# Optimization experiments

Hardware: AMD Instinct MI355X
Metric: run time of the kernel (lower is better)

The kernel has to match this reference:

```python
import jax, jax.numpy as jnp
import numpy as np

STRIDE = 1
PADDING = 1


def _ternarize(w):
    # threshold = 0.75 * mean(|w|); alpha = mean(|w| over |w| > threshold)
    abs_w = jnp.abs(w)
    threshold = 0.75 * jnp.mean(abs_w)
    mask = abs_w > threshold
    cnt = jnp.sum(mask)
    alpha = jnp.where(cnt > 0, jnp.sum(jnp.where(mask, abs_w, 0.0)) / jnp.maximum(cnt, 1), 1.0)
    tern = jnp.where(w > threshold, alpha, jnp.where(w < -threshold, -alpha, 0.0))
    # straight-through estimator: forward uses tern, grad flows to w as identity
    return w + jax.lax.stop_gradient(tern - w)


def setup_inputs() -> dict:
    key = jax.random.key(0)
    k_x, k_w = jax.random.split(key)
    x = jax.random.normal(k_x, (32, 256, 56, 56), dtype=jnp.float32)
    weight = jax.random.normal(k_w, (256, 256, 3, 3), dtype=jnp.float32)
    return {"x": x, "weight": weight}


def reference(x, weight):
    tw = _ternarize(weight)
    # NCHW input, OIHW kernel
    return jax.lax.conv_general_dilated(
        x, tw,
        window_strides=(STRIDE, STRIDE),
        padding=[(PADDING, PADDING), (PADDING, PADDING)],
        dimension_numbers=("NCHW", "OIHW", "NCHW"),
    )
```

## Files before the change

### kernel.cpp

```cpp
#include <hip/hip_runtime.h>
#include <hip/hip_bf16.h>

typedef short short8 __attribute__((ext_vector_type(8)));
typedef float f32x4 __attribute__((ext_vector_type(4)));

constexpr int N_  = 32;
constexpr int C_  = 256;
constexpr int K_  = 256;
constexpr int H_  = 56;
constexpr int W_  = 56;
constexpr int HW_ = H_ * W_;
constexpr int NW_ = K_ * C_ * 9;

constexpr int TH   = 4;
constexpr int NB   = 14;
constexpr int HR   = 6, HC = 58;
constexpr int NH   = HR * HC;
constexpr int BROW = 80;
constexpr int BSZ  = NH * BROW;
constexpr int NPAIR2 = 8 * NH;
constexpr int SITER  = 6;
constexpr int ASTEP  = 16384;

constexpr int WS_P1 = 4, WS_P2 = 260, WS_P3 = 516;
constexpr size_t WS_WQ = 4096;
constexpr size_t WS_NEEDED = WS_WQ + (size_t)NW_ * 2;

__device__ __forceinline__ unsigned f2bf(float f) {
    unsigned u = __builtin_bit_cast(unsigned, f);
    return (u + 0x7FFFu + ((u >> 16) & 1u)) >> 16;
}

__global__ void k_abs_partial(const float* __restrict__ w, float* __restrict__ ws) {
    __shared__ float sm[4];
    float s = 0.f;
    for (int i = blockIdx.x * 256 + threadIdx.x; i < NW_; i += 256 * 256)
        s += fabsf(w[i]);
    #pragma unroll
    for (int o = 32; o > 0; o >>= 1) s += __shfl_down(s, o, 64);
    const int wid = threadIdx.x >> 6, lane = threadIdx.x & 63;
    if (lane == 0) sm[wid] = s;
    __syncthreads();
    if (threadIdx.x == 0) {
        float r = 0.f;
        for (int i = 0; i < 4; ++i) r += sm[i];
        ws[WS_P1 + blockIdx.x] = r;
    }
}

__global__ void k_masked_partial(const float* __restrict__ w, float* __restrict__ ws) {
    __shared__ float sm[4];
    float t = ws[WS_P1 + threadIdx.x];
    #pragma unroll
    for (int o = 32; o > 0; o >>= 1) t += __shfl_down(t, o, 64);
    const int wid = threadIdx.x >> 6, lane = threadIdx.x & 63;
    if (lane == 0) sm[wid] = t;
    __syncthreads();
    float total = 0.f;
    for (int i = 0; i < 4; ++i) total += sm[i];
    const float thr = 0.75f * total / (float)NW_;
    if (blockIdx.x == 0 && threadIdx.x == 0) ws[0] = total;
    __syncthreads();
    float s = 0.f, c = 0.f;
    for (int i = blockIdx.x * 256 + threadIdx.x; i < NW_; i += 256 * 256) {
        float a = fabsf(w[i]);
        if (a > thr) { s += a; c += 1.f; }
    }
    #pragma unroll
    for (int o = 32; o > 0; o >>= 1) { s += __shfl_down(s, o, 64); c += __shfl_down(c, o, 64); }
    __shared__ float sm2[8];
    if (lane == 0) { sm2[wid] = s; sm2[wid + 4] = c; }
    __syncthreads();
    if (threadIdx.x == 0) {
        float S = 0.f, C2 = 0.f;
        for (int i = 0; i < 4; ++i) { S += sm2[i]; C2 += sm2[i + 4]; }
        ws[WS_P2 + blockIdx.x] = S;
        ws[WS_P3 + blockIdx.x] = C2;
    }
}

__global__ void k_final_masked(float* __restrict__ ws) {
    __shared__ float sm[8];
    float s = ws[WS_P2 + threadIdx.x];
    float c = ws[WS_P3 + threadIdx.x];
    #pragma unroll
    for (int o = 32; o > 0; o >>= 1) { s += __shfl_down(s, o, 64); c += __shfl_down(c, o, 64); }
    const int wid = threadIdx.x >> 6, lane = threadIdx.x & 63;
    if (lane == 0) { sm[wid] = s; sm[wid + 4] = c; }
    __syncthreads();
    if (threadIdx.x == 0) {
        float S = 0.f, C2 = 0.f;
        for (int i = 0; i < 4; ++i) { S += sm[i]; C2 += sm[i + 4]; }
        ws[1] = S; ws[2] = C2;
    }
}

__device__ __forceinline__ float reduce256_all(const float* __restrict__ p, float* sm) {
    float v = threadIdx.x < 256 ? p[threadIdx.x] : 0.f;
    #pragma unroll
    for (int o = 32; o > 0; o >>= 1) v += __shfl_down(v, o, 64);
    const int wid = threadIdx.x >> 6, lane = threadIdx.x & 63;
    __syncthreads();
    if (lane == 0) sm[wid] = v;
    __syncthreads();
    float total = 0.f;
    #pragma unroll
    for (int i = 0; i < 8; ++i) total += sm[i];
    return total;
}

__global__ __launch_bounds__(512) void k_quant(const float* __restrict__ w,
                                               float* __restrict__ ws,
                                               unsigned short* __restrict__ wq) {
    __shared__ float sm[8];
    const float total = reduce256_all(ws + WS_P1, sm);
    const float msum  = reduce256_all(ws + WS_P2, sm);
    const float mcnt  = reduce256_all(ws + WS_P3, sm);
    const float thr = 0.75f * total / (float)NW_;
    const float alpha = mcnt > 0.f ? msum / fmaxf(mcnt, 1.f) : 1.0f;
    if (blockIdx.x == 0 && threadIdx.x == 0) ws[3] = alpha;
    const int i = blockIdx.x * 512 + threadIdx.x;
    if (i >= NW_) return;
    const float v = w[i];
    const unsigned short q = v > thr ? (unsigned short)0x3F80
                                     : (v < -thr ? (unsigned short)0xBF80 : (unsigned short)0);
    const int k   = i / 2304;
    const int rem = i - k * 2304;
    const int c   = rem / 9;
    const int rs  = rem - c * 9;
    const int chi = c >> 5, c5 = c & 31;
    wq[(size_t)(chi * 9 + rs) * 8192 + (k << 5) + c5] = q;
}

constexpr int RSO_[9] = {
    (0*HC+0)*BROW, (0*HC+1)*BROW, (0*HC+2)*BROW,
    (1*HC+0)*BROW, (1*HC+1)*BROW, (1*HC+2)*BROW,
    (2*HC+0)*BROW, (2*HC+1)*BROW, (2*HC+2)*BROW };

struct ConvState {
    const float* xn;
    const char*  wqc;
    char*        ldsp;
    size_t       aoff;
    int          tid;
    int          bB[7];
    int          xrel[SITER];
    unsigned     okm;
};

__device__ __forceinline__ void load_a(short8 (&d)[4], const ConvState& st, int step) {
    const char* ap = st.wqc + (size_t)step * ASTEP + st.aoff;
    d[0] = *(const short8*)(ap);
    d[1] = *(const short8*)(ap + 1024);
    d[2] = *(const short8*)(ap + 2048);
    d[3] = *(const short8*)(ap + 3072);
}

__device__ __forceinline__ void issue_b(const ConvState& st, int c0, float (&bs)[SITER][4]) {
    #pragma unroll
    for (int it = 0; it < SITER; ++it) {
        const float* p = st.xn + (size_t)c0 * HW_ + st.xrel[it];
        bs[it][0] = p[0];
        bs[it][1] = p[HW_];
        bs[it][2] = p[2 * HW_];
        bs[it][3] = p[3 * HW_];
    }
}

__device__ __forceinline__ void write_b(const ConvState& st, int base,
                                        const float (&bs)[SITER][4]) {
    #pragma unroll
    for (int it = 0; it < SITER; ++it) {
        const int u = it * 512 + st.tid;
        if (u < NPAIR2) {
            const int c4 = u / NH, hidx = u - c4 * NH;
            const bool ok = (st.okm >> it) & 1u;
            const float f0 = ok ? bs[it][0] : 0.f;
            const float f1 = ok ? bs[it][1] : 0.f;
            const float f2 = ok ? bs[it][2] : 0.f;
            const float f3 = ok ? bs[it][3] : 0.f;
            uint2 v;
            v.x = f2bf(f0) | (f2bf(f1) << 16);
            v.y = f2bf(f2) | (f2bf(f3) << 16);
            *(uint2*)(st.ldsp + base + hidx * BROW + c4 * 8) = v;
        }
    }
}

template <int PAR, bool LASTCH>
__device__ __forceinline__ void do_chunk(int chi, const ConvState& st,
                                         short8 (&afr)[2][4], f32x4 (&acc)[4][7],
                                         float (&bs)[SITER][4]) {
    const int rdbase = PAR * BSZ;
    #pragma unroll
    for (int rs = 0; rs < 9; ++rs) {
        const int cur = (PAR + rs) & 1, nxt = cur ^ 1;
        const int step = chi * 9 + rs;
        if (!(LASTCH && rs == 8))
            load_a(afr[nxt], st, step + 1);

        short8 bfr[7];
        #pragma unroll
        for (int nf = 0; nf < 7; ++nf)
            bfr[nf] = *(const short8*)(st.ldsp + rdbase + st.bB[nf] + RSO_[rs]);

        if (rs == 5 && !LASTCH)
            issue_b(st, (chi + 1) * 32, bs);

        if (rs == 8 && !LASTCH) {
            write_b(st, (PAR ^ 1) * BSZ, bs);
            asm volatile("s_waitcnt lgkmcnt(0)" ::: "memory");
            __builtin_amdgcn_s_barrier();
        }

        __builtin_amdgcn_s_setprio(1);
        #pragma unroll
        for (int nf = 0; nf < 7; ++nf)
            #pragma unroll
            for (int mf = 0; mf < 4; ++mf)
                acc[mf][nf] = __builtin_amdgcn_mfma_f32_16x16x32_bf16(
                    afr[cur][mf], bfr[nf], acc[mf][nf], 0, 0, 0);
        __builtin_amdgcn_s_setprio(0);
    }
}

__global__ __launch_bounds__(512, 2) void conv_mfma(const float* __restrict__ x,
                                                    const unsigned short* __restrict__ wq,
                                                    const float* __restrict__ wsc,
                                                    float* __restrict__ out) {
    __shared__ char lds[2 * BSZ];
    const int tid = threadIdx.x, lane = tid & 63, wid = tid >> 6;
    const int wm = wid & 3, wn = wid >> 2, lr = lane & 15, lg = lane >> 4;
    const int band = blockIdx.x, n = blockIdx.y;
    const int h0 = band * TH;

    ConvState st;
    st.xn   = x + (size_t)n * C_ * HW_;
    st.wqc  = (const char*)wq;
    st.ldsp = lds;
    st.aoff = (size_t)(wm * 64 + lr) * 64 + lg * 16;
    st.tid  = tid;
    #pragma unroll
    for (int nf = 0; nf < 7; ++nf) {
        const int pos = wn * 112 + nf * 16 + lr;
        const int y = pos / 56, xx = pos - y * 56;
        st.bB[nf] = (y * HC + xx) * BROW + lg * 16;
    }
    st.okm = 0;
    #pragma unroll
    for (int it = 0; it < SITER; ++it) {
        const int u  = it * 512 + tid;
        const bool vu = u < NPAIR2;
        const int uu = vu ? u : 0;
        const int c4 = uu / NH, hidx = uu - c4 * NH;
        const int hy = hidx / HC, hx = hidx - hy * HC;
        const int h = h0 - 1 + hy, w = hx - 1;
        const bool ok = vu && (unsigned)h < (unsigned)H_ && (unsigned)w < (unsigned)W_;
        st.xrel[it] = ok ? (4 * c4 * HW_ + h * W_ + w) : 0;
        st.okm |= (ok ? 1u : 0u) << it;
    }

    f32x4 acc[4][7] = {};
    short8 afr[2][4];
    float bs[SITER][4];

    issue_b(st, 0, bs);
    load_a(afr[0], st, 0);
    write_b(st, 0, bs);
    asm volatile("s_waitcnt lgkmcnt(0)" ::: "memory");
    __builtin_amdgcn_s_barrier();

    for (int cc = 0; cc < 3; ++cc) {
        do_chunk<0, false>(2 * cc,     st, afr, acc, bs);
        do_chunk<1, false>(2 * cc + 1, st, afr, acc, bs);
    }
    do_chunk<0, false>(6, st, afr, acc, bs);
    do_chunk<1, true >(7, st, afr, acc, bs);

    const float alpha = wsc[3];
    #pragma unroll
    for (int mf = 0; mf < 4; ++mf) {
        const int kb = wm * 64 + mf * 16 + lg * 4;
        #pragma unroll
        for (int j = 0; j < 4; ++j) {
            float* pk = out + ((size_t)n * K_ + (kb + j)) * HW_ + h0 * W_;
            #pragma unroll
            for (int nf = 0; nf < 7; ++nf) {
                const int pos = wn * 112 + nf * 16 + lr;
                pk[pos] = alpha * acc[mf][nf][j];
            }
        }
    }
}

constexpr int W4_ = W_ / 4;
constexpr int SP_ = H_ * W4_;
__global__ __launch_bounds__(256) void conv_tern_otf(const float* __restrict__ x,
                                                     const float* __restrict__ wt,
                                                     const float* __restrict__ wsc,
                                                     float* __restrict__ out) {
    const int kg = blockIdx.x, n = blockIdx.y, k0 = kg * 4;
    const float thr = 0.75f * wsc[0] / (float)NW_;
    const float cnt = wsc[2];
    const float alpha = cnt > 0.f ? wsc[1] / fmaxf(cnt, 1.f) : 1.0f;
    for (int j = 0; j < 4; ++j) {
        const int sp = (int)threadIdx.x + j * 256;
        if (sp >= SP_) break;
        const int h = sp / W4_, w0 = (sp % W4_) * 4;
        float acc[4][4];
        #pragma unroll
        for (int kt = 0; kt < 4; ++kt)
            #pragma unroll
            for (int jj = 0; jj < 4; ++jj) acc[kt][jj] = 0.f;
        for (int c = 0; c < C_; ++c) {
            const float* xp = x + (((size_t)n * C_ + c) * H_) * W_;
            float xr[3][6];
            #pragma unroll
            for (int r = 0; r < 3; ++r) {
                const int hh = h + r - 1;
                const float* rowp = xp + hh * W_;
                if ((unsigned)hh < (unsigned)H_) {
                    const float4 mid = *(const float4*)(rowp + w0);
                    xr[r][1] = mid.x; xr[r][2] = mid.y; xr[r][3] = mid.z; xr[r][4] = mid.w;
                    xr[r][0] = (w0 > 0)      ? rowp[w0 - 1] : 0.f;
                    xr[r][5] = (w0 + 4 < W_) ? rowp[w0 + 4] : 0.f;
                } else {
                    #pragma unroll
                    for (int q = 0; q < 6; ++q) xr[r][q] = 0.f;
                }
            }
            #pragma unroll
            for (int kt = 0; kt < 4; ++kt) {
                const float* wp = wt + ((size_t)(k0 + kt) * C_ + c) * 9;
                #pragma unroll
                for (int r = 0; r < 3; ++r)
                    #pragma unroll
                    for (int s = 0; s < 3; ++s) {
                        float wv = wp[r * 3 + s];
                        wv = wv > thr ? alpha : (wv < -thr ? -alpha : 0.f);
                        #pragma unroll
                        for (int jj = 0; jj < 4; ++jj)
                            acc[kt][jj] = fmaf(wv, xr[r][jj + s], acc[kt][jj]);
                    }
            }
        }
        #pragma unroll
        for (int kt = 0; kt < 4; ++kt) {
            float4 o;
            o.x = acc[kt][0]; o.y = acc[kt][1]; o.z = acc[kt][2]; o.w = acc[kt][3];
            *(float4*)(out + ((((size_t)n * K_ + (k0 + kt)) * H_ + h) * W_ + w0)) = o;
        }
    }
}

extern "C" void kernel_launch(void* const* d_in, const int* in_sizes, int n_in,
                              void* d_out, int out_size, void* d_ws, size_t ws_size,
                              hipStream_t stream) {
    const float* x = (const float*)d_in[0];
    const float* w = (const float*)d_in[1];
    float* out = (float*)d_out;
    float* ws  = (float*)d_ws;
    unsigned short* wq = (unsigned short*)((char*)d_ws + WS_WQ);

    k_abs_partial<<<256, 256, 0, stream>>>(w, ws);
    k_masked_partial<<<256, 256, 0, stream>>>(w, ws);

    if (ws_size >= WS_NEEDED) {
        k_quant<<<(NW_ + 511) / 512, 512, 0, stream>>>(w, ws, wq);
        dim3 grid(NB, N_);
        conv_mfma<<<grid, 512, 0, stream>>>(x, wq, ws, out);
    } else {
        k_final_masked<<<1, 256, 0, stream>>>(ws);
        dim3 grid(64, N_);
        conv_tern_otf<<<grid, 256, 0, stream>>>(x, w, ws, out);
    }
}
```

Before: 138.6 us.

## Fuse masked stats into quant kernel and quad-buffer conv LDS staging

Removes the separate masked-sum pass by having k_quant compute per-block masked sums and counts while quantizing, and moves the alpha reduction into the conv epilogue. The conv kernel switches to four LDS buffers in dynamic shared memory, staging two chunks ahead and placing a barrier only every other chunk, which cuts synchronization. The output store loop is also reordered. The cost is 4x BSZ of LDS per block (about 111KB), which may hurt occupancy at two blocks per CU, plus a per-launch hipFuncSetAttribute call.

```diff
diff --git a/kernel.cpp b/kernel.cpp
--- a/kernel.cpp
+++ b/kernel.cpp
@@ -18,12 +18,16 @@
 constexpr int NH   = HR * HC;
 constexpr int BROW = 80;
 constexpr int BSZ  = NH * BROW;
+constexpr int LDSB = 4 * BSZ;
 constexpr int NPAIR2 = 8 * NH;
 constexpr int SITER  = 6;
 constexpr int ASTEP  = 16384;
 
-constexpr int WS_P1 = 4, WS_P2 = 260, WS_P3 = 516;
-constexpr size_t WS_WQ = 4096;
+constexpr int NQB   = 1152;
+constexpr int WS_P1 = 4;
+constexpr int WS_P2 = 300;
+constexpr int WS_P3 = 1500;
+constexpr size_t WS_WQ = 16384;
 constexpr size_t WS_NEEDED = WS_WQ + (size_t)NW_ * 2;
 
 __device__ __forceinline__ unsigned f2bf(float f) {
@@ -48,53 +52,6 @@
     }
 }
 
-__global__ void k_masked_partial(const float* __restrict__ w, float* __restrict__ ws) {
-    __shared__ float sm[4];
-    float t = ws[WS_P1 + threadIdx.x];
-    #pragma unroll
-    for (int o = 32; o > 0; o >>= 1) t += __shfl_down(t, o, 64);
-    const int wid = threadIdx.x >> 6, lane = threadIdx.x & 63;
-    if (lane == 0) sm[wid] = t;
-    __syncthreads();
-    float total = 0.f;
-    for (int i = 0; i < 4; ++i) total += sm[i];
-    const float thr = 0.75f * total / (float)NW_;
-    if (blockIdx.x == 0 && threadIdx.x == 0) ws[0] = total;
-    __syncthreads();
-    float s = 0.f, c = 0.f;
-    for (int i = blockIdx.x * 256 + threadIdx.x; i < NW_; i += 256 * 256) {
-        float a = fabsf(w[i]);
-        if (a > thr) { s += a; c += 1.f; }
-    }
-    #pragma unroll
-    for (int o = 32; o > 0; o >>= 1) { s += __shfl_down(s, o, 64); c += __shfl_down(c, o, 64); }
-    __shared__ float sm2[8];
-    if (lane == 0) { sm2[wid] = s; sm2[wid + 4] = c; }
-    __syncthreads();
-    if (threadIdx.x == 0) {
-        float S = 0.f, C2 = 0.f;
-        for (int i = 0; i < 4; ++i) { S += sm2[i]; C2 += sm2[i + 4]; }
-        ws[WS_P2 + blockIdx.x] = S;
-        ws[WS_P3 + blockIdx.x] = C2;
-    }
-}
-
-__global__ void k_final_masked(float* __restrict__ ws) {
-    __shared__ float sm[8];
-    float s = ws[WS_P2 + threadIdx.x];
-    float c = ws[WS_P3 + threadIdx.x];
-    #pragma unroll
-    for (int o = 32; o > 0; o >>= 1) { s += __shfl_down(s, o, 64); c += __shfl_down(c, o, 64); }
-    const int wid = threadIdx.x >> 6, lane = threadIdx.x & 63;
-    if (lane == 0) { sm[wid] = s; sm[wid + 4] = c; }
-    __syncthreads();
-    if (threadIdx.x == 0) {
-        float S = 0.f, C2 = 0.f;
-        for (int i = 0; i < 4; ++i) { S += sm[i]; C2 += sm[i + 4]; }
-        ws[1] = S; ws[2] = C2;
-    }
-}
-
 __device__ __forceinline__ float reduce256_all(const float* __restrict__ p, float* sm) {
     float v = threadIdx.x < 256 ? p[threadIdx.x] : 0.f;
     #pragma unroll
@@ -114,13 +71,8 @@
                                                unsigned short* __restrict__ wq) {
     __shared__ float sm[8];
     const float total = reduce256_all(ws + WS_P1, sm);
-    const float msum  = reduce256_all(ws + WS_P2, sm);
-    const float mcnt  = reduce256_all(ws + WS_P3, sm);
     const float thr = 0.75f * total / (float)NW_;
-    const float alpha = mcnt > 0.f ? msum / fmaxf(mcnt, 1.f) : 1.0f;
-    if (blockIdx.x == 0 && threadIdx.x == 0) ws[3] = alpha;
     const int i = blockIdx.x * 512 + threadIdx.x;
-    if (i >= NW_) return;
     const float v = w[i];
     const unsigned short q = v > thr ? (unsigned short)0x3F80
                                      : (v < -thr ? (unsigned short)0xBF80 : (unsigned short)0);
@@ -130,6 +82,74 @@
     const int rs  = rem - c * 9;
     const int chi = c >> 5, c5 = c & 31;
     wq[(size_t)(chi * 9 + rs) * 8192 + (k << 5) + c5] = q;
+    const float a = fabsf(v);
+    float s = a > thr ? a : 0.f;
+    float cn = a > thr ? 1.f : 0.f;
+    #pragma unroll
+    for (int o = 32; o > 0; o >>= 1) { s += __shfl_down(s, o, 64); cn += __shfl_down(cn, o, 64); }
+    __shared__ float sm2[16];
+    const int wid = threadIdx.x >> 6, lane = threadIdx.x & 63;
+    __syncthreads();
+    if (lane == 0) { sm2[wid] = s; sm2[8 + wid] = cn; }
+    __syncthreads();
+    if (threadIdx.x == 0) {
+        float S = 0.f, C2 = 0.f;
+        for (int j = 0; j < 8; ++j) { S += sm2[j]; C2 += sm2[8 + j]; }
+        ws[WS_P2 + blockIdx.x] = S;
+        ws[WS_P3 + blockIdx.x] = C2;
+    }
+}
+
+__global__ void k_fb_total(float* __restrict__ ws) {
+    __shared__ float sm[4];
+    float v = ws[WS_P1 + threadIdx.x];
+    #pragma unroll
+    for (int o = 32; o > 0; o >>= 1) v += __shfl_down(v, o, 64);
+    const int wid = threadIdx.x >> 6, lane = threadIdx.x & 63;
+    if (lane == 0) sm[wid] = v;
+    __syncthreads();
+    if (threadIdx.x == 0) {
+        float r = 0.f;
+        for (int i = 0; i < 4; ++i) r += sm[i];
+        ws[0] = r;
+    }
+}
+
+__global__ void k_fb_masked(const float* __restrict__ w, float* __restrict__ ws) {
+    const float thr = 0.75f * ws[0] / (float)NW_;
+    float s = 0.f, c = 0.f;
+    for (int i = blockIdx.x * 256 + threadIdx.x; i < NW_; i += 256 * 256) {
+        float a = fabsf(w[i]);
+        if (a > thr) { s += a; c += 1.f; }
+    }
+    #pragma unroll
+    for (int o = 32; o > 0; o >>= 1) { s += __shfl_down(s, o, 64); c += __shfl_down(c, o, 64); }
+    __shared__ float sm[8];
+    const int wid = threadIdx.x >> 6, lane = threadIdx.x & 63;
+    if (lane == 0) { sm[wid] = s; sm[4 + wid] = c; }
+    __syncthreads();
+    if (threadIdx.x == 0) {
+        float S = 0.f, C2 = 0.f;
+        for (int i = 0; i < 4; ++i) { S += sm[i]; C2 += sm[i + 4]; }
+        ws[WS_P2 + blockIdx.x] = S;
+        ws[WS_P3 + blockIdx.x] = C2;
+    }
+}
+
+__global__ void k_final_masked(float* __restrict__ ws) {
+    __shared__ float sm[8];
+    float s = ws[WS_P2 + threadIdx.x];
+    float c = ws[WS_P3 + threadIdx.x];
+    #pragma unroll
+    for (int o = 32; o > 0; o >>= 1) { s += __shfl_down(s, o, 64); c += __shfl_down(c, o, 64); }
+    const int wid = threadIdx.x >> 6, lane = threadIdx.x & 63;
+    if (lane == 0) { sm[wid] = s; sm[4 + wid] = c; }
+    __syncthreads();
+    if (threadIdx.x == 0) {
+        float S = 0.f, C2 = 0.f;
+        for (int i = 0; i < 4; ++i) { S += sm[i]; C2 += sm[i + 4]; }
+        ws[1] = S; ws[2] = C2;
+    }
 }
 
 constexpr int RSO_[9] = {
@@ -187,11 +207,14 @@
     }
 }
 
-template <int PAR, bool LASTCH>
+template <int BUF, bool STAGE, bool BAR>
 __device__ __forceinline__ void do_chunk(int chi, const ConvState& st,
                                          short8 (&afr)[2][4], f32x4 (&acc)[4][7],
                                          float (&bs)[SITER][4]) {
-    const int rdbase = PAR * BSZ;
+    constexpr int PAR    = BUF & 1;
+    constexpr int rdbase = BUF * BSZ;
+    constexpr int wrbase = ((BUF + 2) & 3) * BSZ;
+    constexpr bool LASTCH = (BUF == 3) && !STAGE && !BAR;
     #pragma unroll
     for (int rs = 0; rs < 9; ++rs) {
         const int cur = (PAR + rs) & 1, nxt = cur ^ 1;
@@ -204,14 +227,8 @@
         for (int nf = 0; nf < 7; ++nf)
             bfr[nf] = *(const short8*)(st.ldsp + rdbase + st.bB[nf] + RSO_[rs]);
 
-        if (rs == 5 && !LASTCH)
-            issue_b(st, (chi + 1) * 32, bs);
-
-        if (rs == 8 && !LASTCH) {
-            write_b(st, (PAR ^ 1) * BSZ, bs);
-            asm volatile("s_waitcnt lgkmcnt(0)" ::: "memory");
-            __builtin_amdgcn_s_barrier();
-        }
+        if (STAGE && rs == 6)
+            issue_b(st, (chi + 2) * 32, bs);
 
         __builtin_amdgcn_s_setprio(1);
         #pragma unroll
@@ -221,6 +238,14 @@
                 acc[mf][nf] = __builtin_amdgcn_mfma_f32_16x16x32_bf16(
                     afr[cur][mf], bfr[nf], acc[mf][nf], 0, 0, 0);
         __builtin_amdgcn_s_setprio(0);
+
+        if (rs == 8) {
+            if (STAGE) write_b(st, wrbase, bs);
+            if (BAR) {
+                asm volatile("s_waitcnt lgkmcnt(0)" ::: "memory");
+                __builtin_amdgcn_s_barrier();
+            }
+        }
     }
 }
 
@@ -228,7 +253,7 @@
                                                     const unsigned short* __restrict__ wq,
                                                     const float* __restrict__ wsc,
                                                     float* __restrict__ out) {
-    __shared__ char lds[2 * BSZ];
+    extern __shared__ char lds[];
     const int tid = threadIdx.x, lane = tid & 63, wid = tid >> 6;
     const int wm = wid & 3, wn = wid >> 2, lr = lane & 15, lg = lane >> 4;
     const int band = blockIdx.x, n = blockIdx.y;
@@ -264,31 +289,51 @@
     short8 afr[2][4];
     float bs[SITER][4];
 
+    load_a(afr[0], st, 0);
     issue_b(st, 0, bs);
-    load_a(afr[0], st, 0);
-    write_b(st, 0, bs);
+    write_b(st, 0 * BSZ, bs);
+    issue_b(st, 32, bs);
+    write_b(st, 1 * BSZ, bs);
     asm volatile("s_waitcnt lgkmcnt(0)" ::: "memory");
     __builtin_amdgcn_s_barrier();
 
-    for (int cc = 0; cc < 3; ++cc) {
-        do_chunk<0, false>(2 * cc,     st, afr, acc, bs);
-        do_chunk<1, false>(2 * cc + 1, st, afr, acc, bs);
-    }
-    do_chunk<0, false>(6, st, afr, acc, bs);
-    do_chunk<1, true >(7, st, afr, acc, bs);
-
-    const float alpha = wsc[3];
+    do_chunk<0, true,  false>(0, st, afr, acc, bs);
+    do_chunk<1, true,  true >(1, st, afr, acc, bs);
+    do_chunk<2, true,  false>(2, st, afr, acc, bs);
+    do_chunk<3, true,  true >(3, st, afr, acc, bs);
+    do_chunk<0, true,  false>(4, st, afr, acc, bs);
+    do_chunk<1, true,  true >(5, st, afr, acc, bs);
+    do_chunk<2, false, false>(6, st, afr, acc, bs);
+    do_chunk<3, false, false>(7, st, afr, acc, bs);
+
+    __syncthreads();
+    float* sred = (float*)lds;
+    float s2 = wsc[WS_P2 + tid] + wsc[WS_P2 + 512 + tid];
+    float s3 = wsc[WS_P3 + tid] + wsc[WS_P3 + 512 + tid];
+    if (tid < NQB - 1024) {
+        s2 += wsc[WS_P2 + 1024 + tid];
+        s3 += wsc[WS_P3 + 1024 + tid];
+    }
+    #pragma unroll
+    for (int o = 32; o > 0; o >>= 1) { s2 += __shfl_down(s2, o, 64); s3 += __shfl_down(s3, o, 64); }
+    if (lane == 0) { sred[wid] = s2; sred[8 + wid] = s3; }
+    __syncthreads();
+    float msum = 0.f, mcnt = 0.f;
+    #pragma unroll
+    for (int i = 0; i < 8; ++i) { msum += sred[i]; mcnt += sred[8 + i]; }
+    const float alpha = mcnt > 0.f ? msum / fmaxf(mcnt, 1.f) : 1.0f;
+
     #pragma unroll
     for (int mf = 0; mf < 4; ++mf) {
-        const int kb = wm * 64 + mf * 16 + lg * 4;
+        const int k = wm * 64 + mf * 16 + lg * 4;
         #pragma unroll
-        for (int j = 0; j < 4; ++j) {
-            float* pk = out + ((size_t)n * K_ + (kb + j)) * HW_ + h0 * W_;
+        for (int nf = 0; nf < 7; ++nf) {
+            const int pos = wn * 112 + nf * 16 + lr;
+            const int y = pos / 56, xx = pos - y * 56;
+            float* po = out + ((size_t)n * K_ + k) * HW_ + (h0 + y) * W_ + xx;
             #pragma unroll
-            for (int nf = 0; nf < 7; ++nf) {
-                const int pos = wn * 112 + nf * 16 + lr;
-                pk[pos] = alpha * acc[mf][nf][j];
-            }
+            for (int j = 0; j < 4; ++j)
+                po[(size_t)j * HW_] = alpha * acc[mf][nf][j];
         }
     }
 }
@@ -363,13 +408,16 @@
     unsigned short* wq = (unsigned short*)((char*)d_ws + WS_WQ);
 
     k_abs_partial<<<256, 256, 0, stream>>>(w, ws);
-    k_masked_partial<<<256, 256, 0, stream>>>(w, ws);
 
     if (ws_size >= WS_NEEDED) {
-        k_quant<<<(NW_ + 511) / 512, 512, 0, stream>>>(w, ws, wq);
+        k_quant<<<NQB, 512, 0, stream>>>(w, ws, wq);
+        hipFuncSetAttribute((const void*)conv_mfma,
+                            hipFuncAttributeMaxDynamicSharedMemorySize, LDSB);
         dim3 grid(NB, N_);
-        conv_mfma<<<grid, 512, 0, stream>>>(x, wq, ws, out);
+        conv_mfma<<<grid, 512, LDSB, stream>>>(x, wq, ws, out);
     } else {
+        k_fb_total<<<1, 256, 0, stream>>>(ws);
+        k_fb_masked<<<256, 256, 0, stream>>>(w, ws);
         k_final_masked<<<1, 256, 0, stream>>>(ws);
         dim3 grid(64, N_);
         conv_tern_otf<<<grid, 256, 0, stream>>>(x, w, ws, out);
```

Result: slower. 144.0 us (+3.8%).
